# Optimization experiments

Measured on AMD Instinct MI355X. Metric: run time of the kernel, lower is better.

Reference implementation:

```python
import jax, jax.numpy as jnp
import numpy as np

B, C, T, Fd = 4, 256, 64, 256
H = 8
HID = int(C * 2.0)
LN_EPS = 1e-5
L2_EPS = 1e-12


def _layernorm(x, g, b):
    mu = jnp.mean(x, axis=-1, keepdims=True)
    var = jnp.mean((x - mu) ** 2, axis=-1, keepdims=True)
    return (x - mu) * jax.lax.rsqrt(var + LN_EPS) * g + b


def _l2norm(x):
    n = jnp.sqrt(jnp.sum(x * x, axis=-1, keepdims=True))
    return x / jnp.maximum(n, L2_EPS)


def setup_inputs() -> dict:
    key = jax.random.key(0)
    ks = jax.random.split(key, 8)
    s = 0.02
    return {
        "x": jax.random.normal(ks[0], (B, C, T, Fd), dtype=jnp.float32),
        "norm1_g": jnp.ones((C,), jnp.float32),
        "norm1_b": jnp.zeros((C,), jnp.float32),
        "Wqkv": jax.random.normal(ks[1], (C, 3 * C), jnp.float32) * s,
        "dw_w": jax.random.normal(ks[2], (3 * C, 1, 3), jnp.float32) * s,  # depthwise conv1d kernel (O, I/g=1, K)
        "Wproj": jax.random.normal(ks[3], (C, C), jnp.float32) * s,
        "temperature": jnp.full((H, 1, 1), 0.5, jnp.float32),
        "norm2_g": jnp.ones((C,), jnp.float32),
        "norm2_b": jnp.zeros((C,), jnp.float32),
        "W1": jax.random.normal(ks[4], (C, HID), jnp.float32) * s,
        "b1": jnp.zeros((HID,), jnp.float32),
        "W2": jax.random.normal(ks[5], (HID, C), jnp.float32) * s,
        "b2": jnp.zeros((C,), jnp.float32),
    }


def reference(x, norm1_g, norm1_b, Wqkv, dw_w, Wproj, temperature,
              norm2_g, norm2_b, W1, b1, W2, b2):
    b, c, t, f = x.shape
    # axis='freq': (b c t f) -> ((b t) f c)
    xs = jnp.transpose(x, (0, 2, 3, 1)).reshape(b * t, f, c)

    xn = _layernorm(xs, norm1_g, norm1_b)
    qkv = xn @ Wqkv                                  # (bt, f, 3c)
    # depthwise conv1d along the sequence (freq) axis, kernel 3, pad 1
    qkv = jnp.transpose(qkv, (0, 2, 1))              # (bt, 3c, f)
    qkv = jax.lax.conv_general_dilated(
        qkv, dw_w, window_strides=(1,), padding=[(1, 1)],
        feature_group_count=3 * c,
        dimension_numbers=("NCH", "OIH", "NCH"))
    qkv = jnp.transpose(qkv, (0, 2, 1))              # (bt, f, 3c)

    q, k, v = jnp.split(qkv, 3, axis=-1)
    d = c // H
    def heads(z):  # (bt, s, c) -> (bt, h, s, d)
        return jnp.transpose(z.reshape(b * t, f, H, d), (0, 2, 1, 3))
    q, k, v = heads(q), heads(k), heads(v)

    q = _l2norm(q)
    k = _l2norm(k)
    attn = jnp.einsum("bhsd,bhtd->bhst", q, k) * temperature  # temp broadcasts (h,1,1)
    attn = jax.nn.softmax(attn, axis=-1)
    out = jnp.einsum("bhst,bhtd->bhsd", attn, v)
    out = jnp.transpose(out, (0, 2, 1, 3)).reshape(b * t, f, c)
    out = out @ Wproj
    out = out + xs

    h = _layernorm(out, norm2_g, norm2_b)
    h = jax.nn.gelu(h @ W1 + b1, approximate=False) @ W2 + b2
    out = out + h

    # ((b t) f c) -> (b c t f)
    out = out.reshape(b, t, f, c)
    return jnp.transpose(out, (0, 3, 1, 2))
```

## Files before the change

kernel.cpp:

```cpp
#include <hip/hip_runtime.h>
#include <math.h>

#define Bv 4
#define Cv 256
#define Tv 64
#define Fv 256
#define Hv 8
#define HIDv 512
#define Mv 65536
#define CTF (Cv * Tv * Fv)
#define TF (Tv * Fv)

typedef unsigned short u16;
typedef __attribute__((ext_vector_type(8))) short bfx8;
typedef __attribute__((ext_vector_type(4))) float f32x4;

__device__ __forceinline__ float bf2f(u16 u) {
  return __uint_as_float(((unsigned int)u) << 16);
}
__device__ __forceinline__ u16 f2bf(float f) {
  unsigned int x = __float_as_uint(f);
  unsigned int r = x + 0x7fffu + ((x >> 16) & 1u);
  return (u16)(r >> 16);
}
__device__ __forceinline__ unsigned int cvtpk(float a, float b) {
  unsigned int r;
  asm("v_cvt_pk_bf16_f32 %0, %1, %2" : "=v"(r) : "v"(a), "v"(b));
  return r;
}

__launch_bounds__(256)
__global__ void transpose_w(const float* __restrict__ in, u16* __restrict__ out,
                            int K, int N) {
  __shared__ float t[32][33];
  const int n0 = blockIdx.x * 32, k0 = blockIdx.y * 32;
  const int c = threadIdx.x & 31, r = threadIdx.x >> 5;
#pragma unroll
  for (int i = 0; i < 4; ++i)
    t[r + 8 * i][c] = in[(size_t)(k0 + r + 8 * i) * N + n0 + c];
  __syncthreads();
#pragma unroll
  for (int i = 0; i < 4; ++i)
    out[(size_t)(n0 + r + 8 * i) * K + k0 + c] = f2bf(t[c][r + 8 * i]);
}

__launch_bounds__(256)
__global__ void ln1_kernel(const float* __restrict__ x, const float* __restrict__ g,
                           const float* __restrict__ bta, u16* __restrict__ xn) {
  __shared__ float tile[256][33];
  __shared__ float red1[8][32];
  __shared__ float red2[8][32];
  __shared__ float mu_s[32];
  __shared__ float rs_s[32];
  const int tid = threadIdx.x;
  const int blk = blockIdx.x;
  const int n = blk >> 3;
  const int f0 = (blk & 7) << 5;
  const int bb = n >> 6, tt = n & 63;
  const float* xb = x + (size_t)bb * CTF + (size_t)tt * Fv;
  const int fl = tid & 31, c0 = tid >> 5;
#pragma unroll
  for (int i = 0; i < 32; ++i) {
    int c = i * 8 + c0;
    tile[c][fl] = xb[(size_t)c * TF + f0 + fl];
  }
  __syncthreads();
  const int col = tid & 31, part = tid >> 5;
  float s = 0.f, s2 = 0.f;
#pragma unroll
  for (int i = 0; i < 32; ++i) {
    float v = tile[part * 32 + i][col];
    s += v; s2 += v * v;
  }
  red1[part][col] = s; red2[part][col] = s2;
  __syncthreads();
  if (tid < 32) {
    float S1 = 0.f, S2 = 0.f;
#pragma unroll
    for (int p = 0; p < 8; ++p) { S1 += red1[p][tid]; S2 += red2[p][tid]; }
    float m = S1 * (1.f / 256.f);
    float var = S2 * (1.f / 256.f) - m * m;
    mu_s[tid] = m;
    rs_s[tid] = rsqrtf(var + 1e-5f);
  }
  __syncthreads();
  const float gv = g[tid], bv = bta[tid];
  u16* ob = xn + ((size_t)n * 256 + f0) * 256 + tid;
#pragma unroll
  for (int fl2 = 0; fl2 < 32; ++fl2) {
    ob[(size_t)fl2 * 256] = f2bf((tile[tid][fl2] - mu_s[fl2]) * rs_s[fl2] * gv + bv);
  }
}

template <int K, int N, int EPI>
__launch_bounds__(256)
__global__ void gemm_mfma(const u16* __restrict__ A, const u16* __restrict__ Bt,
                          void* __restrict__ Cc, const float* __restrict__ aux0,
                          const u16* __restrict__ aux1) {
  constexpr int GX = N / 128;
  constexpr bool SWAP = (EPI == 0 || EPI == 2);
  __shared__ u16 As[128 * 64];
  __shared__ u16 Bs[128 * 64];
  const int tid = threadIdx.x;
  const int lane = tid & 63, wid = tid >> 6;
  int id = blockIdx.y * GX + blockIdx.x;
  const int qch = (GX * gridDim.y) >> 3;
  id = (id & 7) * qch + (id >> 3);
  const int m0 = (id / GX) * 128, n0 = (id % GX) * 128;
  const int wm = (wid & 1) * 64, wn = (wid >> 1) * 64;
  const int lm = lane & 15, quad = lane >> 4;

  const int l8 = lane >> 3, c8 = lane & 7;
  const int gc = (c8 ^ l8) * 8;

  f32x4 acc[4][4] = {};
  for (int k0 = 0; k0 < K; k0 += 64) {
    __syncthreads();
#pragma unroll
    for (int i = 0; i < 4; ++i) {
      const int rb = wid * 32 + i * 8;
      const int row = rb + l8;
      __builtin_amdgcn_global_load_lds(
          (const __attribute__((address_space(1))) void*)(A + (size_t)(m0 + row) * K + k0 + gc),
          (__attribute__((address_space(3))) void*)(&As[rb * 64]), 16, 0, 0);
      __builtin_amdgcn_global_load_lds(
          (const __attribute__((address_space(1))) void*)(Bt + (size_t)(n0 + row) * K + k0 + gc),
          (__attribute__((address_space(3))) void*)(&Bs[rb * 64]), 16, 0, 0);
    }
    __syncthreads();
#pragma unroll
    for (int s = 0; s < 2; ++s) {
      bfx8 af[4], bf[4];
#pragma unroll
      for (int t = 0; t < 4; ++t) {
        const int ra = wm + t * 16 + lm;
        const int rbr = wn + t * 16 + lm;
        af[t] = *(const bfx8*)&As[ra * 64 + (((s * 4 + quad) ^ (ra & 7))) * 8];
        bf[t] = *(const bfx8*)&Bs[rbr * 64 + (((s * 4 + quad) ^ (rbr & 7))) * 8];
      }
#pragma unroll
      for (int tm = 0; tm < 4; ++tm)
#pragma unroll
        for (int tn = 0; tn < 4; ++tn) {
          if constexpr (SWAP)
            acc[tm][tn] = __builtin_amdgcn_mfma_f32_16x16x32_bf16(bf[tn], af[tm], acc[tm][tn], 0, 0, 0);
          else
            acc[tm][tn] = __builtin_amdgcn_mfma_f32_16x16x32_bf16(af[tm], bf[tn], acc[tm][tn], 0, 0, 0);
        }
    }
  }

  if constexpr (SWAP) {
#pragma unroll
    for (int tm = 0; tm < 4; ++tm) {
      const int grow = m0 + wm + tm * 16 + lm;
#pragma unroll
      for (int tn = 0; tn < 4; ++tn) {
        const int gcol0 = n0 + wn + tn * 16 + quad * 4;
        u16* dst = (u16*)Cc + (size_t)grow * N + gcol0;
        if constexpr (EPI == 0) {
          uint2 pk;
          pk.x = cvtpk(acc[tm][tn][0], acc[tm][tn][1]);
          pk.y = cvtpk(acc[tm][tn][2], acc[tm][tn][3]);
          *(uint2*)dst = pk;
        } else {
          const float4 b4 = *(const float4*)(aux0 + gcol0);
          float o[4];
#pragma unroll
          for (int r = 0; r < 4; ++r) {
            float v = acc[tm][tn][r] + ((const float*)&b4)[r];
            float y = 0.79788456080286536f * (v + 0.044715f * v * v * v);
            float th = 1.f - 2.f / (__expf(2.f * y) + 1.f);
            o[r] = 0.5f * v * (1.f + th);
          }
          uint2 pk;
          pk.x = cvtpk(o[0], o[1]);
          pk.y = cvtpk(o[2], o[3]);
          *(uint2*)dst = pk;
        }
      }
    }
  } else {
    const int row_l = quad * 4;
    const int nn = m0 >> 8;
    const int bb = nn >> 6, tt = nn & 63;
    const int srow_base = (m0 & 255) + wm;
    float bcol[4];
    if constexpr (EPI == 3) {
#pragma unroll
      for (int tn = 0; tn < 4; ++tn) bcol[tn] = aux0[n0 + wn + tn * 16 + lm];
    }
#pragma unroll
    for (int tm = 0; tm < 4; ++tm) {
      const int grow0 = m0 + wm + tm * 16 + row_l;
      const int sr0 = srow_base + tm * 16 + row_l;
#pragma unroll
      for (int tn = 0; tn < 4; ++tn) {
        const int gcol = n0 + wn + tn * 16 + lm;
        if constexpr (EPI == 1) {
          const float4 xv = *(const float4*)(aux0 + (size_t)bb * CTF + (size_t)gcol * TF + tt * Fv + sr0);
          const float xr[4] = {xv.x, xv.y, xv.z, xv.w};
#pragma unroll
          for (int r = 0; r < 4; ++r)
            ((u16*)Cc)[(size_t)(grow0 + r) * N + gcol] = f2bf(acc[tm][tn][r] + xr[r]);
        } else {
          float4 o;
#pragma unroll
          for (int r = 0; r < 4; ++r) {
            float res = bf2f(aux1[(size_t)(grow0 + r) * 256 + gcol]);
            ((float*)&o)[r] = acc[tm][tn][r] + bcol[tn] + res;
          }
          *(float4*)((float*)Cc + (size_t)bb * CTF + (size_t)gcol * TF + tt * Fv + sr0) = o;
        }
      }
    }
  }
}

__launch_bounds__(512)
__global__ void attn_kernel(const u16* __restrict__ qkv, const float* __restrict__ dw,
                            const float* __restrict__ temp, u16* __restrict__ attn_out) {
  __shared__ u16 Kc[2][64 * 40];
  __shared__ u16 Vt[2][32 * 72];
  __shared__ float l_s[256];
  const int tid = threadIdx.x;
  const int lane = tid & 63, w = tid >> 6;
  const int l15 = lane & 15, quad = lane >> 4;
  const int n = blockIdx.x >> 3, h = blockIdx.x & 7;
  const int h32 = h * 32;
  const u16* base = qkv + (size_t)n * 256 * 768;
  const float th2 = temp[h] * 1.44269504089f;

  bfx8 bq[2];
  {
    const int d0q = quad * 8;
    float wq[3][8];
#pragma unroll
    for (int j = 0; j < 8; ++j)
#pragma unroll
      for (int t = 0; t < 3; ++t) wq[t][j] = dw[(h32 + d0q + j) * 3 + t];
#pragma unroll
    for (int ct = 0; ct < 2; ++ct) {
      const int row = w * 32 + ct * 16 + l15;
      const u16* src = base + (size_t)row * 768 + h32 + d0q;
      float v[8];
      const bfx8 bm = *(const bfx8*)src;
#pragma unroll
      for (int j = 0; j < 8; ++j) v[j] = wq[1][j] * bf2f((u16)bm[j]);
      if (row > 0) {
        const bfx8 bp = *(const bfx8*)(src - 768);
#pragma unroll
        for (int j = 0; j < 8; ++j) v[j] += wq[0][j] * bf2f((u16)bp[j]);
      }
      if (row < 255) {
        const bfx8 bn = *(const bfx8*)(src + 768);
#pragma unroll
        for (int j = 0; j < 8; ++j) v[j] += wq[2][j] * bf2f((u16)bn[j]);
      }
      float ssq = 0.f;
#pragma unroll
      for (int j = 0; j < 8; ++j) ssq += v[j] * v[j];
      ssq += __shfl_xor(ssq, 16);
      ssq += __shfl_xor(ssq, 32);
      const float inv = 1.f / fmaxf(sqrtf(ssq), 1e-12f);
      union { unsigned int u[4]; bfx8 b; } qb;
#pragma unroll
      for (int m = 0; m < 4; ++m) qb.u[m] = cvtpk(v[2 * m] * inv, v[2 * m + 1] * inv);
      bq[ct] = qb.b;
    }
  }

  const bool isK = tid < 256;
  const int sV = tid & 255;
  const int krow = sV >> 2, kd0 = (sV & 3) * 8;
  const int vd = sV & 31, vko = sV >> 5;
  float wu[24];
  if (isK) {
#pragma unroll
    for (int j = 0; j < 8; ++j)
#pragma unroll
      for (int t = 0; t < 3; ++t) wu[t * 8 + j] = dw[(256 + h32 + kd0 + j) * 3 + t];
  } else {
#pragma unroll
    for (int t = 0; t < 3; ++t) wu[t] = dw[(512 + h32 + vd) * 3 + t];
  }

  bfx8 km = {}, kp = {}, kn = {};
  u16 xs[10];

  auto stage_load = [&](int c) {
    if (isK) {
      const int gr = c * 64 + krow;
      const u16* src = base + (size_t)gr * 768 + 256 + h32 + kd0;
      km = *(const bfx8*)src;
      kp = (gr > 0) ? *(const bfx8*)(src - 768) : bfx8{};
      kn = (gr < 255) ? *(const bfx8*)(src + 768) : bfx8{};
    } else {
      const int g0 = c * 64 + vko * 8;
      const u16* src = base + (size_t)g0 * 768 + 512 + h32 + vd;
#pragma unroll
      for (int k = 0; k < 10; ++k) {
        const int gr = g0 + k - 1;
        xs[k] = (gr >= 0 && gr < 256) ? src[(ptrdiff_t)(k - 1) * 768] : (u16)0;
      }
    }
  };
  auto stage_finish = [&](int b) {
    if (isK) {
      float v[8];
#pragma unroll
      for (int j = 0; j < 8; ++j)
        v[j] = wu[8 + j] * bf2f((u16)km[j]) + wu[j] * bf2f((u16)kp[j]) +
               wu[16 + j] * bf2f((u16)kn[j]);
      float ssq = 0.f;
#pragma unroll
      for (int j = 0; j < 8; ++j) ssq += v[j] * v[j];
      ssq += __shfl_xor(ssq, 1);
      ssq += __shfl_xor(ssq, 2);
      const float inv = 1.f / fmaxf(sqrtf(ssq), 1e-12f);
      union { unsigned int u[4]; bfx8 b; } kb;
#pragma unroll
      for (int m = 0; m < 4; ++m) kb.u[m] = cvtpk(v[2 * m] * inv, v[2 * m + 1] * inv);
      *(bfx8*)&Kc[b][krow * 40 + kd0] = kb.b;
    } else {
      float x[10];
#pragma unroll
      for (int k = 0; k < 10; ++k) x[k] = bf2f(xs[k]);
      union { unsigned int u[4]; bfx8 b; } ob;
#pragma unroll
      for (int m = 0; m < 4; ++m) {
        float a0 = wu[0] * x[2 * m] + wu[1] * x[2 * m + 1] + wu[2] * x[2 * m + 2];
        float a1 = wu[0] * x[2 * m + 1] + wu[1] * x[2 * m + 2] + wu[2] * x[2 * m + 3];
        ob.u[m] = cvtpk(a0, a1);
      }
      const int po = vko ^ ((vd >> 3) & 3);
      *(bfx8*)&Vt[b][vd * 72 + po * 8] = ob.b;
    }
  };

  f32x4 acc[2][2] = {};
  float lsum[2] = {0.f, 0.f};
  const f32x4 zf = {0.f, 0.f, 0.f, 0.f};
  const int fo = (l15 >> 3) & 1;

  stage_load(0);
  stage_finish(0);
  __syncthreads();

  for (int c = 0; c < 4; ++c) {
    const int b = c & 1;
    if (c < 3) stage_load(c + 1);

    bfx8 af[4];
#pragma unroll
    for (int rt = 0; rt < 4; ++rt)
      af[rt] = *(const bfx8*)&Kc[b][(rt * 16 + l15) * 40 + quad * 8];
#pragma unroll
    for (int ct = 0; ct < 2; ++ct) {
      unsigned int pu[4], pv[4];
#pragma unroll
      for (int rt = 0; rt < 4; ++rt) {
        f32x4 sc = __builtin_amdgcn_mfma_f32_16x16x32_bf16(af[rt], bq[ct], zf, 0, 0, 0);
        float e0 = exp2f(sc[0] * th2), e1 = exp2f(sc[1] * th2);
        float e2 = exp2f(sc[2] * th2), e3 = exp2f(sc[3] * th2);
        lsum[ct] += (e0 + e1) + (e2 + e3);
        pu[rt] = cvtpk(e0, e1);
        pv[rt] = cvtpk(e2, e3);
      }
#pragma unroll
      for (int ks = 0; ks < 2; ++ks) {
        auto su = __builtin_amdgcn_permlane32_swap(pu[2 * ks], pu[2 * ks + 1], false, false);
        auto tu = __builtin_amdgcn_permlane16_swap(su[0], su[1], false, false);
        auto sv = __builtin_amdgcn_permlane32_swap(pv[2 * ks], pv[2 * ks + 1], false, false);
        auto tv = __builtin_amdgcn_permlane16_swap(sv[0], sv[1], false, false);
        union { unsigned int u[4]; bfx8 b; } ap;
        ap.u[0] = tu[0]; ap.u[1] = tv[0]; ap.u[2] = tu[1]; ap.u[3] = tv[1];
        const bfx8 bv0 = *(const bfx8*)&Vt[b][l15 * 72 + (ks * 4 + (quad ^ fo)) * 8];
        const bfx8 bv1 = *(const bfx8*)&Vt[b][(16 + l15) * 72 + (ks * 4 + (quad ^ (2 | fo))) * 8];
        acc[ct][0] = __builtin_amdgcn_mfma_f32_16x16x32_bf16(ap.b, bv0, acc[ct][0], 0, 0, 0);
        acc[ct][1] = __builtin_amdgcn_mfma_f32_16x16x32_bf16(ap.b, bv1, acc[ct][1], 0, 0, 0);
      }
    }
    if (c < 3) stage_finish(b ^ 1);
    __syncthreads();
  }

#pragma unroll
  for (int ct = 0; ct < 2; ++ct) {
    float L = lsum[ct];
    L += __shfl_xor(L, 16);
    L += __shfl_xor(L, 32);
    if (quad == 0) l_s[w * 32 + ct * 16 + l15] = L;
  }
#pragma unroll
  for (int ct = 0; ct < 2; ++ct) {
    const f32x4 l4 = *(const f32x4*)&l_s[w * 32 + ct * 16 + quad * 4];
    float rinv[4];
#pragma unroll
    for (int r = 0; r < 4; ++r) rinv[r] = 1.f / l4[r];
#pragma unroll
    for (int dh = 0; dh < 2; ++dh)
#pragma unroll
      for (int r = 0; r < 4; ++r) {
        const int qrow = w * 32 + ct * 16 + quad * 4 + r;
        attn_out[((size_t)n * 256 + qrow) * 256 + h32 + dh * 16 + l15] =
            f2bf(acc[ct][dh][r] * rinv[r]);
      }
  }
}

__launch_bounds__(256)
__global__ void ln2_kernel(const u16* __restrict__ in, const float* __restrict__ g,
                           const float* __restrict__ bta, u16* __restrict__ out) {
  const int lane = threadIdx.x & 63;
  const size_t row = (size_t)blockIdx.x * 4 + (threadIdx.x >> 6);
  const ushort4 u = ((const ushort4*)(in + row * 256))[lane];
  const float vx = bf2f(u.x), vy = bf2f(u.y), vz = bf2f(u.z), vw = bf2f(u.w);
  float s = vx + vy + vz + vw;
  float s2 = vx * vx + vy * vy + vz * vz + vw * vw;
#pragma unroll
  for (int m = 32; m >= 1; m >>= 1) {
    s += __shfl_xor(s, m, 64);
    s2 += __shfl_xor(s2, m, 64);
  }
  const float mu = s * (1.f / 256.f);
  const float rs = rsqrtf(s2 * (1.f / 256.f) - mu * mu + 1e-5f);
  const float4 gv = ((const float4*)g)[lane];
  const float4 bv = ((const float4*)bta)[lane];
  ushort4 o;
  o.x = f2bf((vx - mu) * rs * gv.x + bv.x);
  o.y = f2bf((vy - mu) * rs * gv.y + bv.y);
  o.z = f2bf((vz - mu) * rs * gv.z + bv.z);
  o.w = f2bf((vw - mu) * rs * gv.w + bv.w);
  ((ushort4*)(out + row * 256))[lane] = o;
}

extern "C" void kernel_launch(void* const* d_in, const int* in_sizes, int n_in,
                              void* d_out, int out_size, void* d_ws, size_t ws_size,
                              hipStream_t stream) {
  const float* x     = (const float*)d_in[0];
  const float* n1g   = (const float*)d_in[1];
  const float* n1b   = (const float*)d_in[2];
  const float* Wqkv  = (const float*)d_in[3];
  const float* dw    = (const float*)d_in[4];
  const float* Wproj = (const float*)d_in[5];
  const float* temp  = (const float*)d_in[6];
  const float* n2g   = (const float*)d_in[7];
  const float* n2b   = (const float*)d_in[8];
  const float* W1    = (const float*)d_in[9];
  const float* b1    = (const float*)d_in[10];
  const float* W2    = (const float*)d_in[11];
  const float* b2    = (const float*)d_in[12];

  char* ws = (char*)d_ws;
  u16* xn       = (u16*)(ws);
  u16* qkv      = (u16*)(ws + (32ull << 20));
  u16* attn_out = xn;
  u16* out1     = (u16*)(ws + (32ull << 20));
  u16* xn2      = xn;
  u16* h1       = (u16*)(ws + (64ull << 20));
  u16* w2t      = xn;

  char* ob = (char*)d_out;
  u16* wqkvt  = (u16*)(ob);
  u16* wprojt = (u16*)(ob + (1ull << 20));
  u16* w1t    = (u16*)(ob + 1572864ull);

  transpose_w<<<dim3(24, 8), 256, 0, stream>>>(Wqkv, wqkvt, 256, 768);
  transpose_w<<<dim3(8, 8), 256, 0, stream>>>(Wproj, wprojt, 256, 256);
  transpose_w<<<dim3(16, 8), 256, 0, stream>>>(W1, w1t, 256, 512);

  ln1_kernel<<<2048, 256, 0, stream>>>(x, n1g, n1b, xn);
  gemm_mfma<256, 768, 0><<<dim3(6, 512), 256, 0, stream>>>(xn, wqkvt, qkv, nullptr, nullptr);
  attn_kernel<<<2048, 512, 0, stream>>>(qkv, dw, temp, attn_out);
  gemm_mfma<256, 256, 1><<<dim3(2, 512), 256, 0, stream>>>(attn_out, wprojt, out1, x, nullptr);
  ln2_kernel<<<16384, 256, 0, stream>>>(out1, n2g, n2b, xn2);
  gemm_mfma<256, 512, 2><<<dim3(4, 512), 256, 0, stream>>>(xn2, W1 ? w1t : w1t, h1, b1, nullptr);
  transpose_w<<<dim3(8, 16), 256, 0, stream>>>(W2, w2t, 512, 256);
  gemm_mfma<512, 256, 3><<<dim3(2, 512), 256, 0, stream>>>(h1, w2t, d_out, b2, out1);
}
```

Before: 427.0 us.

## Fuse projection GEMM, residual add and LayerNorm2 into one kernel

Adds a projection GEMM kernel whose block tile spans a full 256-wide row (128x256). Its epilogue adds the residual from x, reduces row mean and variance across waves, and writes both out1 and the normalized xn2. This removes the separate ln2 kernel and its extra read and write of out1. In exchange each thread holds a larger accumulator and the grid has only 512 blocks, which may reduce occupancy and latency hiding. The unused residual epilogue path is also dropped from the generic GEMM.

```diff
diff --git a/kernel.cpp b/kernel.cpp
--- a/kernel.cpp
+++ b/kernel.cpp
@@ -186,10 +186,8 @@
     const int bb = nn >> 6, tt = nn & 63;
     const int srow_base = (m0 & 255) + wm;
     float bcol[4];
-    if constexpr (EPI == 3) {
-#pragma unroll
-      for (int tn = 0; tn < 4; ++tn) bcol[tn] = aux0[n0 + wn + tn * 16 + lm];
-    }
+#pragma unroll
+    for (int tn = 0; tn < 4; ++tn) bcol[tn] = aux0[n0 + wn + tn * 16 + lm];
 #pragma unroll
     for (int tm = 0; tm < 4; ++tm) {
       const int grow0 = m0 + wm + tm * 16 + row_l;
@@ -197,22 +195,139 @@
 #pragma unroll
       for (int tn = 0; tn < 4; ++tn) {
         const int gcol = n0 + wn + tn * 16 + lm;
-        if constexpr (EPI == 1) {
-          const float4 xv = *(const float4*)(aux0 + (size_t)bb * CTF + (size_t)gcol * TF + tt * Fv + sr0);
-          const float xr[4] = {xv.x, xv.y, xv.z, xv.w};
-#pragma unroll
-          for (int r = 0; r < 4; ++r)
-            ((u16*)Cc)[(size_t)(grow0 + r) * N + gcol] = f2bf(acc[tm][tn][r] + xr[r]);
-        } else {
-          float4 o;
-#pragma unroll
-          for (int r = 0; r < 4; ++r) {
-            float res = bf2f(aux1[(size_t)(grow0 + r) * 256 + gcol]);
-            ((float*)&o)[r] = acc[tm][tn][r] + bcol[tn] + res;
-          }
-          *(float4*)((float*)Cc + (size_t)bb * CTF + (size_t)gcol * TF + tt * Fv + sr0) = o;
+        float4 o;
+#pragma unroll
+        for (int r = 0; r < 4; ++r) {
+          float res = bf2f(aux1[(size_t)(grow0 + r) * 256 + gcol]);
+          ((float*)&o)[r] = acc[tm][tn][r] + bcol[tn] + res;
         }
-      }
+        *(float4*)((float*)Cc + (size_t)bb * CTF + (size_t)gcol * TF + tt * Fv + sr0) = o;
+      }
+    }
+  }
+}
+
+__launch_bounds__(256)
+__global__ void gemm_proj_ln(const u16* __restrict__ A, const u16* __restrict__ Bt,
+                             const float* __restrict__ x, const float* __restrict__ g,
+                             const float* __restrict__ bta,
+                             u16* __restrict__ out1, u16* __restrict__ xn2) {
+  __shared__ u16 As[128 * 64];
+  __shared__ u16 Bs[256 * 64];
+  __shared__ float red1[2][128];
+  __shared__ float red2[2][128];
+  __shared__ float muS[128];
+  __shared__ float rsS[128];
+  const int tid = threadIdx.x;
+  const int lane = tid & 63, wid = tid >> 6;
+  int id = blockIdx.x;
+  id = (id & 7) * 64 + (id >> 3);
+  const int m0 = id * 128;
+  const int wm = (wid & 1) * 64, wn = (wid >> 1) * 128;
+  const int lm = lane & 15, quad = lane >> 4;
+  const int l8 = lane >> 3, c8 = lane & 7;
+  const int gc = (c8 ^ l8) * 8;
+
+  f32x4 acc[4][8] = {};
+  for (int k0 = 0; k0 < 256; k0 += 64) {
+    __syncthreads();
+#pragma unroll
+    for (int i = 0; i < 4; ++i) {
+      const int rb = wid * 32 + i * 8;
+      const int row = rb + l8;
+      __builtin_amdgcn_global_load_lds(
+          (const __attribute__((address_space(1))) void*)(A + (size_t)(m0 + row) * 256 + k0 + gc),
+          (__attribute__((address_space(3))) void*)(&As[rb * 64]), 16, 0, 0);
+    }
+#pragma unroll
+    for (int i = 0; i < 8; ++i) {
+      const int rb = wid * 64 + i * 8;
+      const int row = rb + l8;
+      __builtin_amdgcn_global_load_lds(
+          (const __attribute__((address_space(1))) void*)(Bt + (size_t)row * 256 + k0 + gc),
+          (__attribute__((address_space(3))) void*)(&Bs[rb * 64]), 16, 0, 0);
+    }
+    __syncthreads();
+#pragma unroll
+    for (int s = 0; s < 2; ++s) {
+      bfx8 af[4], bf[8];
+#pragma unroll
+      for (int t = 0; t < 4; ++t) {
+        const int ra = wm + t * 16 + lm;
+        af[t] = *(const bfx8*)&As[ra * 64 + (((s * 4 + quad) ^ (ra & 7))) * 8];
+      }
+#pragma unroll
+      for (int t = 0; t < 8; ++t) {
+        const int rb2 = wn + t * 16 + lm;
+        bf[t] = *(const bfx8*)&Bs[rb2 * 64 + (((s * 4 + quad) ^ (rb2 & 7))) * 8];
+      }
+#pragma unroll
+      for (int tm = 0; tm < 4; ++tm)
+#pragma unroll
+        for (int tn = 0; tn < 8; ++tn)
+          acc[tm][tn] = __builtin_amdgcn_mfma_f32_16x16x32_bf16(bf[tn], af[tm], acc[tm][tn], 0, 0, 0);
+    }
+  }
+
+  const int nn = m0 >> 8;
+  const int bb = nn >> 6, tt = nn & 63;
+  const int fbase = (m0 & 255) + wm;
+  float s1[4] = {}, s2v[4] = {};
+#pragma unroll
+  for (int tm = 0; tm < 4; ++tm) {
+    const int f = fbase + tm * 16 + lm;
+    const float* xr = x + (size_t)bb * CTF + (size_t)tt * Fv + f;
+#pragma unroll
+    for (int tn = 0; tn < 8; ++tn) {
+      const int gcol0 = wn + tn * 16 + quad * 4;
+#pragma unroll
+      for (int j = 0; j < 4; ++j) {
+        float v = acc[tm][tn][j] + xr[(size_t)(gcol0 + j) * TF];
+        acc[tm][tn][j] = v;
+        s1[tm] += v; s2v[tm] += v * v;
+      }
+    }
+  }
+#pragma unroll
+  for (int tm = 0; tm < 4; ++tm) {
+    s1[tm] += __shfl_xor(s1[tm], 16);  s1[tm] += __shfl_xor(s1[tm], 32);
+    s2v[tm] += __shfl_xor(s2v[tm], 16); s2v[tm] += __shfl_xor(s2v[tm], 32);
+  }
+  if (quad == 0) {
+#pragma unroll
+    for (int tm = 0; tm < 4; ++tm) {
+      red1[wid >> 1][wm + tm * 16 + lm] = s1[tm];
+      red2[wid >> 1][wm + tm * 16 + lm] = s2v[tm];
+    }
+  }
+  __syncthreads();
+  if (tid < 128) {
+    const float S = red1[0][tid] + red1[1][tid];
+    const float Q = red2[0][tid] + red2[1][tid];
+    const float mu = S * (1.f / 256.f);
+    muS[tid] = mu;
+    rsS[tid] = rsqrtf(Q * (1.f / 256.f) - mu * mu + 1e-5f);
+  }
+  __syncthreads();
+#pragma unroll
+  for (int tm = 0; tm < 4; ++tm) {
+    const int lrow = wm + tm * 16 + lm;
+    const int grow = m0 + lrow;
+    const float mu = muS[lrow], rs = rsS[lrow];
+#pragma unroll
+    for (int tn = 0; tn < 8; ++tn) {
+      const int gcol0 = wn + tn * 16 + quad * 4;
+      const float4 g4 = *(const float4*)(g + gcol0);
+      const float4 b4 = *(const float4*)(bta + gcol0);
+      const float o0 = acc[tm][tn][0], o1 = acc[tm][tn][1];
+      const float o2 = acc[tm][tn][2], o3 = acc[tm][tn][3];
+      uint2 po, pl;
+      po.x = cvtpk(o0, o1);
+      po.y = cvtpk(o2, o3);
+      pl.x = cvtpk((o0 - mu) * rs * g4.x + b4.x, (o1 - mu) * rs * g4.y + b4.y);
+      pl.y = cvtpk((o2 - mu) * rs * g4.z + b4.z, (o3 - mu) * rs * g4.w + b4.w);
+      *(uint2*)(out1 + (size_t)grow * 256 + gcol0) = po;
+      *(uint2*)(xn2 + (size_t)grow * 256 + gcol0) = pl;
     }
   }
 }
@@ -407,32 +522,6 @@
             f2bf(acc[ct][dh][r] * rinv[r]);
       }
   }
-}
-
-__launch_bounds__(256)
-__global__ void ln2_kernel(const u16* __restrict__ in, const float* __restrict__ g,
-                           const float* __restrict__ bta, u16* __restrict__ out) {
-  const int lane = threadIdx.x & 63;
-  const size_t row = (size_t)blockIdx.x * 4 + (threadIdx.x >> 6);
-  const ushort4 u = ((const ushort4*)(in + row * 256))[lane];
-  const float vx = bf2f(u.x), vy = bf2f(u.y), vz = bf2f(u.z), vw = bf2f(u.w);
-  float s = vx + vy + vz + vw;
-  float s2 = vx * vx + vy * vy + vz * vz + vw * vw;
-#pragma unroll
-  for (int m = 32; m >= 1; m >>= 1) {
-    s += __shfl_xor(s, m, 64);
-    s2 += __shfl_xor(s2, m, 64);
-  }
-  const float mu = s * (1.f / 256.f);
-  const float rs = rsqrtf(s2 * (1.f / 256.f) - mu * mu + 1e-5f);
-  const float4 gv = ((const float4*)g)[lane];
-  const float4 bv = ((const float4*)bta)[lane];
-  ushort4 o;
-  o.x = f2bf((vx - mu) * rs * gv.x + bv.x);
-  o.y = f2bf((vy - mu) * rs * gv.y + bv.y);
-  o.z = f2bf((vz - mu) * rs * gv.z + bv.z);
-  o.w = f2bf((vw - mu) * rs * gv.w + bv.w);
-  ((ushort4*)(out + row * 256))[lane] = o;
 }
 
 extern "C" void kernel_launch(void* const* d_in, const int* in_sizes, int n_in,
@@ -473,8 +562,7 @@
   ln1_kernel<<<2048, 256, 0, stream>>>(x, n1g, n1b, xn);
   gemm_mfma<256, 768, 0><<<dim3(6, 512), 256, 0, stream>>>(xn, wqkvt, qkv, nullptr, nullptr);
   attn_kernel<<<2048, 512, 0, stream>>>(qkv, dw, temp, attn_out);
-  gemm_mfma<256, 256, 1><<<dim3(2, 512), 256, 0, stream>>>(attn_out, wprojt, out1, x, nullptr);
-  ln2_kernel<<<16384, 256, 0, stream>>>(out1, n2g, n2b, xn2);
+  gemm_proj_ln<<<512, 256, 0, stream>>>(attn_out, wprojt, x, n2g, n2b, out1, xn2);
   gemm_mfma<256, 512, 2><<<dim3(4, 512), 256, 0, stream>>>(xn2, W1 ? w1t : w1t, h1, b1, nullptr);
   transpose_w<<<dim3(8, 16), 256, 0, stream>>>(W2, w2t, 512, 256);
   gemm_mfma<512, 256, 3><<<dim3(2, 512), 256, 0, stream>>>(h1, w2t, d_out, b2, out1);
```

Measured after the change: 436.3 us. 1.02x slower.
